# Optimization experiments

Measured on AMD Instinct MI355X. Metric: run time of the kernel, lower is better.

The kernel has to match this reference:

```python
import jax, jax.numpy as jnp
import numpy as np

N_NODES = 50000
N_EDGES = 800000
H_DIM = 128
N_REL2 = 130  # 2 * n_rel with n_rel = 65
BN_EPS = 1e-5


def setup_inputs() -> dict:
    key = jax.random.key(0)
    k1, k2, k3, k4, k5, k6 = jax.random.split(key, 6)
    xavier = float(np.sqrt(2.0 / (H_DIM + H_DIM)))  # xavier_normal_ std for [h,h]
    return {
        "ent_emb": jax.random.normal(k1, (N_NODES, H_DIM), dtype=jnp.float32),
        "rel_emb": jax.random.normal(k2, (N_REL2, H_DIM), dtype=jnp.float32),
        "neigh_w": jax.random.normal(k3, (H_DIM, H_DIM), dtype=jnp.float32) * xavier,
        "gamma": jnp.ones((H_DIM,), dtype=jnp.float32),
        "beta": jnp.zeros((H_DIM,), dtype=jnp.float32),
        "src": jax.random.randint(k4, (N_EDGES,), 0, N_NODES, dtype=jnp.int32),
        "dst": jax.random.randint(k5, (N_EDGES,), 0, N_NODES, dtype=jnp.int32),
        "rel_id": jax.random.randint(k6, (N_EDGES,), 0, N_REL2, dtype=jnp.int32),
    }


def reference(ent_emb, rel_emb, neigh_w, gamma, beta, src, dst, rel_id):
    N = ent_emb.shape[0]
    # u_mul_e: per-edge composition  [E, h]
    comp = ent_emb[src] * rel_emb[rel_id]
    # e_dot_v: per-edge attention logit  [E]
    score = jnp.sum(comp * ent_emb[dst], axis=-1)
    # edge_softmax over incoming edges of each dst node (segment softmax)
    seg_max = jax.ops.segment_max(score, dst, num_segments=N)  # [N]
    ex = jnp.exp(score - seg_max[dst])
    denom = jax.ops.segment_sum(ex, dst, num_segments=N)       # [N]
    alpha = ex / denom[dst]                                     # [E]
    # weighted copy_e + sum aggregation to dst nodes  [N, h]
    neigh = jax.ops.segment_sum(comp * alpha[:, None], dst, num_segments=N)
    # dense epilogue: matmul + BatchNorm1d (training-mode batch stats) + tanh
    h = neigh @ neigh_w
    mu = jnp.mean(h, axis=0)
    var = jnp.mean((h - mu) ** 2, axis=0)  # biased variance, as torch BN uses
    h = (h - mu) / jnp.sqrt(var + BN_EPS) * gamma + beta
    return jnp.tanh(h)
```

## Files before the change

kernel.cpp:

```cpp
#include <hip/hip_runtime.h>
#include <hip/hip_fp16.h>
#include <math.h>

#define N_NODES 50000
#define N_EDGES 800000
#define HD 128
#define BN_EPS 1e-5f

#define SCAN_CHUNK 1024
#define SCAN_NB ((N_NODES + SCAN_CHUNK - 1) / SCAN_CHUNK)

typedef __attribute__((ext_vector_type(8))) _Float16 half8;
typedef __attribute__((ext_vector_type(4))) _Float16 h4;
typedef __attribute__((ext_vector_type(4))) float f32x4;

__device__ __forceinline__ unsigned short f2h(float f) {
  return __half_as_ushort(__float2half(f));
}

__global__ __launch_bounds__(256) void conv_w(const float* __restrict__ W,
                                              unsigned short* __restrict__ Wt) {
  __shared__ float sT[32][33];
  int k0 = (blockIdx.x >> 2) * 32, c0 = (blockIdx.x & 3) * 32;
  int tid = threadIdx.x;
  int kk = tid >> 3, cq = tid & 7;
  float4 v = ((const float4*)W)[(k0 + kk) * 32 + (c0 >> 2) + cq];
  sT[kk][cq * 4 + 0] = v.x;
  sT[kk][cq * 4 + 1] = v.y;
  sT[kk][cq * 4 + 2] = v.z;
  sT[kk][cq * 4 + 3] = v.w;
  __syncthreads();
  int cc = tid >> 3, kq = tid & 7;
  h4 o;
  o.x = (_Float16)sT[kq * 4 + 0][cc];
  o.y = (_Float16)sT[kq * 4 + 1][cc];
  o.z = (_Float16)sT[kq * 4 + 2][cc];
  o.w = (_Float16)sT[kq * 4 + 3][cc];
  ((h4*)(Wt + (c0 + cc) * HD + k0))[kq] = o;
}

__global__ __launch_bounds__(256) void hist(const int* __restrict__ dst,
                                            int* __restrict__ counts,
                                            unsigned short* __restrict__ erank) {
  int i = blockIdx.x * 256 + threadIdx.x;
  if (i >= N_EDGES / 4) return;
  int4 d = ((const int4*)dst)[i];
  ushort4 r;
  r.x = (unsigned short)atomicAdd(counts + d.x, 1);
  r.y = (unsigned short)atomicAdd(counts + d.y, 1);
  r.z = (unsigned short)atomicAdd(counts + d.z, 1);
  r.w = (unsigned short)atomicAdd(counts + d.w, 1);
  ((ushort4*)erank)[i] = r;
}

__global__ __launch_bounds__(256) void scan_blocks(
    const int* __restrict__ buf, int* __restrict__ bsum) {
  int t = threadIdx.x;
  int idx = blockIdx.x * SCAN_CHUNK + t * 4;
  int s = 0;
  if (idx + 3 < N_NODES) {
    int4 v = *(const int4*)(buf + idx);
    s = v.x + v.y + v.z + v.w;
  } else {
#pragma unroll
    for (int j = 0; j < 4; ++j)
      if (idx + j < N_NODES) s += buf[idx + j];
  }
  __shared__ int ls[256];
  ls[t] = s;
  __syncthreads();
  for (int off = 128; off > 0; off >>= 1) {
    if (t < off) ls[t] += ls[t + off];
    __syncthreads();
  }
  if (t == 0) bsum[blockIdx.x] = ls[0];
}

__global__ __launch_bounds__(64) void scan_top(const int* __restrict__ bsum,
                                               int* __restrict__ bbase,
                                               int* buf) {
  int t = threadIdx.x;
  int v = (t < SCAN_NB) ? bsum[t] : 0;
  int incl = v;
#pragma unroll
  for (int off = 1; off < 64; off <<= 1) {
    int u = __shfl_up(incl, off, 64);
    if (t >= off) incl += u;
  }
  if (t < SCAN_NB) bbase[t] = incl - v;
  if (t == 63) buf[N_NODES] = incl;
}

__global__ __launch_bounds__(256) void scan_write(int* buf,
                                                  const int* __restrict__ bbase) {
  int t = threadIdx.x;
  int idx = blockIdx.x * SCAN_CHUNK + t * 4;
  int c[4] = {0, 0, 0, 0};
  if (idx + 3 < N_NODES) {
    int4 v = *(const int4*)(buf + idx);
    c[0] = v.x; c[1] = v.y; c[2] = v.z; c[3] = v.w;
  } else {
#pragma unroll
    for (int j = 0; j < 4; ++j)
      if (idx + j < N_NODES) c[j] = buf[idx + j];
  }
  int s = c[0] + c[1] + c[2] + c[3];
  __shared__ int ls[256];
  ls[t] = s;
  __syncthreads();
  for (int off = 1; off < 256; off <<= 1) {
    int u = (t >= off) ? ls[t - off] : 0;
    __syncthreads();
    ls[t] += u;
    __syncthreads();
  }
  int run = bbase[blockIdx.x] + ls[t] - s;
#pragma unroll
  for (int j = 0; j < 4; ++j) {
    if (idx + j < N_NODES) {
      buf[idx + j] = run;
      run += c[j];
    }
  }
}

__global__ __launch_bounds__(256) void fill_buckets(
    const int* __restrict__ src, const int* __restrict__ dst,
    const int* __restrict__ rid, const unsigned short* __restrict__ erank,
    const int* __restrict__ offsets, int* __restrict__ einfo) {
  int i = blockIdx.x * 256 + threadIdx.x;
  if (i >= N_EDGES / 4) return;
  int4 s4 = ((const int4*)src)[i];
  int4 d4 = ((const int4*)dst)[i];
  int4 r4 = ((const int4*)rid)[i];
  ushort4 k4 = ((const ushort4*)erank)[i];
#pragma unroll
  for (int q = 0; q < 4; ++q) {
    int s = (q == 0) ? s4.x : (q == 1) ? s4.y : (q == 2) ? s4.z : s4.w;
    int d = (q == 0) ? d4.x : (q == 1) ? d4.y : (q == 2) ? d4.z : d4.w;
    int r = (q == 0) ? r4.x : (q == 1) ? r4.y : (q == 2) ? r4.z : r4.w;
    int k = (q == 0) ? k4.x : (q == 1) ? k4.y : (q == 2) ? k4.z : k4.w;
    einfo[offsets[d] + k] = s | (r << 16);
  }
}

__global__ __launch_bounds__(256) void gather_fused(
    const float* __restrict__ ent, const float* __restrict__ rel,
    const int* __restrict__ offsets, const int* __restrict__ einfo,
    unsigned short* __restrict__ scaled_h) {
  int n = blockIdx.x * 4 + (threadIdx.x >> 6);
  if (n >= N_NODES) return;
  int lane = threadIdx.x & 63;
  int half = lane >> 5;
  int l32 = lane & 31;
  int s0 = __builtin_amdgcn_readfirstlane(offsets[n]);
  int s1 = __builtin_amdgcn_readfirstlane(offsets[n + 1]);
  const float4* ent4 = (const float4*)ent;
  const float4* rel4 = (const float4*)rel;
  float4 b = ent4[(long)n * 32 + l32];
  const int* ei = einfo + half;

  float m = -INFINITY, den = 0.f;
  float4 acc = make_float4(0.f, 0.f, 0.f, 0.f);
  int s = s0;
  for (; s + 8 <= s1; s += 8) {
    int w0 = ei[s + 0];
    int w1 = ei[s + 2];
    int w2 = ei[s + 4];
    int w3 = ei[s + 6];
    float4 a0 = ent4[(long)(w0 & 0xFFFF) * 32 + l32];
    float4 c0 = rel4[(w0 >> 16) * 32 + l32];
    float4 a1 = ent4[(long)(w1 & 0xFFFF) * 32 + l32];
    float4 c1 = rel4[(w1 >> 16) * 32 + l32];
    float4 a2 = ent4[(long)(w2 & 0xFFFF) * 32 + l32];
    float4 c2 = rel4[(w2 >> 16) * 32 + l32];
    float4 a3 = ent4[(long)(w3 & 0xFFFF) * 32 + l32];
    float4 c3 = rel4[(w3 >> 16) * 32 + l32];
    float4 q0, q1, q2, q3;
    q0.x = a0.x * c0.x; q0.y = a0.y * c0.y; q0.z = a0.z * c0.z; q0.w = a0.w * c0.w;
    q1.x = a1.x * c1.x; q1.y = a1.y * c1.y; q1.z = a1.z * c1.z; q1.w = a1.w * c1.w;
    q2.x = a2.x * c2.x; q2.y = a2.y * c2.y; q2.z = a2.z * c2.z; q2.w = a2.w * c2.w;
    q3.x = a3.x * c3.x; q3.y = a3.y * c3.y; q3.z = a3.z * c3.z; q3.w = a3.w * c3.w;
    float p0 = q0.x * b.x + q0.y * b.y + q0.z * b.z + q0.w * b.w;
    float p1 = q1.x * b.x + q1.y * b.y + q1.z * b.z + q1.w * b.w;
    float p2 = q2.x * b.x + q2.y * b.y + q2.z * b.z + q2.w * b.w;
    float p3 = q3.x * b.x + q3.y * b.y + q3.z * b.z + q3.w * b.w;
#pragma unroll
    for (int off = 16; off > 0; off >>= 1) {
      p0 += __shfl_xor(p0, off, 64);
      p1 += __shfl_xor(p1, off, 64);
      p2 += __shfl_xor(p2, off, 64);
      p3 += __shfl_xor(p3, off, 64);
    }
    float pm = fmaxf(fmaxf(fmaxf(p0, p1), fmaxf(p2, p3)), m);
    float f = __expf(m - pm);
    float e0 = __expf(p0 - pm);
    float e1 = __expf(p1 - pm);
    float e2 = __expf(p2 - pm);
    float e3 = __expf(p3 - pm);
    den = den * f + ((e0 + e1) + (e2 + e3));
    acc.x = acc.x * f + (q0.x * e0 + q1.x * e1) + (q2.x * e2 + q3.x * e3);
    acc.y = acc.y * f + (q0.y * e0 + q1.y * e1) + (q2.y * e2 + q3.y * e3);
    acc.z = acc.z * f + (q0.z * e0 + q1.z * e1) + (q2.z * e2 + q3.z * e3);
    acc.w = acc.w * f + (q0.w * e0 + q1.w * e1) + (q2.w * e2 + q3.w * e3);
    m = pm;
  }
  for (; s + 2 <= s1; s += 2) {
    int w = ei[s];
    float4 a = ent4[(long)(w & 0xFFFF) * 32 + l32];
    float4 c = rel4[(w >> 16) * 32 + l32];
    float4 q;
    q.x = a.x * c.x; q.y = a.y * c.y; q.z = a.z * c.z; q.w = a.w * c.w;
    float p = q.x * b.x + q.y * b.y + q.z * b.z + q.w * b.w;
#pragma unroll
    for (int off = 16; off > 0; off >>= 1) p += __shfl_xor(p, off, 64);
    float pm = fmaxf(p, m);
    float f = __expf(m - pm);
    float e = __expf(p - pm);
    den = den * f + e;
    acc.x = fmaf(acc.x, f, q.x * e);
    acc.y = fmaf(acc.y, f, q.y * e);
    acc.z = fmaf(acc.z, f, q.z * e);
    acc.w = fmaf(acc.w, f, q.w * e);
    m = pm;
  }
  if (s < s1) {
    int w = einfo[s];
    float4 a = ent4[(long)(w & 0xFFFF) * 32 + l32];
    float4 c = rel4[(w >> 16) * 32 + l32];
    float4 q;
    q.x = a.x * c.x; q.y = a.y * c.y; q.z = a.z * c.z; q.w = a.w * c.w;
    float p = q.x * b.x + q.y * b.y + q.z * b.z + q.w * b.w;
#pragma unroll
    for (int off = 16; off > 0; off >>= 1) p += __shfl_xor(p, off, 64);
    float pn = half ? -INFINITY : p;
    float pm = fmaxf(m, pn);
    float f = (m == -INFINITY) ? 0.f : __expf(m - pm);
    float e = (pn == -INFINITY) ? 0.f : __expf(pn - pm);
    den = den * f + e;
    acc.x = fmaf(acc.x, f, q.x * e);
    acc.y = fmaf(acc.y, f, q.y * e);
    acc.z = fmaf(acc.z, f, q.z * e);
    acc.w = fmaf(acc.w, f, q.w * e);
    m = pm;
  }
  float mo = __shfl_xor(m, 32, 64);
  float deno = __shfl_xor(den, 32, 64);
  float4 acco;
  acco.x = __shfl_xor(acc.x, 32, 64);
  acco.y = __shfl_xor(acc.y, 32, 64);
  acco.z = __shfl_xor(acc.z, 32, 64);
  acco.w = __shfl_xor(acc.w, 32, 64);
  float mm = fmaxf(m, mo);
  float fs = (mm == -INFINITY) ? 0.f : __expf(m - mm);
  float fo = (mm == -INFINITY) ? 0.f : __expf(mo - mm);
  float dtot = den * fs + deno * fo;
  float inv = dtot > 0.f ? 1.f / dtot : 0.f;
  if (half == 0) {
    ushort4 o;
    o.x = f2h((acc.x * fs + acco.x * fo) * inv);
    o.y = f2h((acc.y * fs + acco.y * fo) * inv);
    o.z = f2h((acc.z * fs + acco.z * fo) * inv);
    o.w = f2h((acc.w * fs + acco.w * fo) * inv);
    ((ushort4*)(scaled_h + (long)n * HD))[l32] = o;
  }
}

__global__ __launch_bounds__(256) void gemm_mfma(
    const unsigned short* __restrict__ scaled_h,
    const unsigned short* __restrict__ Wt, float* __restrict__ h,
    float* __restrict__ colsum, float* __restrict__ colsumsq) {
  __shared__ unsigned short sW[128 * 136];
  __shared__ float sStat[256];
  int tid = threadIdx.x;
  int row0 = blockIdx.x * 64;

  for (int i = tid; i < 2048; i += 256) {
    int col = i >> 4, c8 = i & 15;
    *(int4*)&sW[col * 136 + c8 * 8] = ((const int4*)Wt)[i];
  }
  __syncthreads();

  int w = tid >> 6, lane = tid & 63;
  int lrow = lane & 15, lk = lane >> 4;
  int arow = row0 + w * 16 + lrow;
  bool avalid = arow < N_NODES;
  const half8* ap = (const half8*)(scaled_h + (long)(avalid ? arow : 0) * HD);

  f32x4 acc[8];
#pragma unroll
  for (int n = 0; n < 8; ++n) acc[n] = (f32x4){0.f, 0.f, 0.f, 0.f};

#pragma unroll
  for (int kt = 0; kt < 4; ++kt) {
    half8 aF = avalid ? ap[kt * 4 + lk]
                      : (half8){(_Float16)0, (_Float16)0, (_Float16)0, (_Float16)0,
                                (_Float16)0, (_Float16)0, (_Float16)0, (_Float16)0};
#pragma unroll
    for (int n = 0; n < 8; ++n) {
      half8 bF = *(const half8*)&sW[(n * 16 + lrow) * 136 + kt * 32 + lk * 8];
      acc[n] = __builtin_amdgcn_mfma_f32_16x16x32_f16(aF, bF, acc[n], 0, 0, 0);
    }
  }

  float s[8], q[8];
#pragma unroll
  for (int n = 0; n < 8; ++n) {
    int col = n * 16 + lrow;
    s[n] = 0.f;
    q[n] = 0.f;
#pragma unroll
    for (int r = 0; r < 4; ++r) {
      float v = acc[n][r];
      int grow = row0 + w * 16 + lk * 4 + r;
      if (grow < N_NODES) h[(long)grow * HD + col] = v;
      s[n] += v;
      q[n] += v * v;
    }
    s[n] += __shfl_xor(s[n], 16, 64);
    s[n] += __shfl_xor(s[n], 32, 64);
    q[n] += __shfl_xor(q[n], 16, 64);
    q[n] += __shfl_xor(q[n], 32, 64);
  }

  sStat[tid] = 0.f;
  __syncthreads();
  if (lane < 16) {
#pragma unroll
    for (int n = 0; n < 8; ++n) {
      atomicAdd(&sStat[n * 16 + lrow], s[n]);
      atomicAdd(&sStat[128 + n * 16 + lrow], q[n]);
    }
  }
  __syncthreads();
  if (tid < 128) {
    unsafeAtomicAdd(colsum + tid, sStat[tid]);
    unsafeAtomicAdd(colsumsq + tid, sStat[128 + tid]);
  }
}

__global__ __launch_bounds__(256) void bn_tanh(
    float* __restrict__ h, const float* __restrict__ colsum,
    const float* __restrict__ colsumsq, const float* __restrict__ gamma,
    const float* __restrict__ beta) {
  const float invN = 1.f / (float)N_NODES;
  const int total4 = N_NODES * 32;
  for (int i = blockIdx.x * 256 + threadIdx.x; i < total4;
       i += gridDim.x * 256) {
    int c4 = i & 31;
    float4 hv = ((float4*)h)[i];
    float4 S = ((const float4*)colsum)[c4];
    float4 Q = ((const float4*)colsumsq)[c4];
    float4 G = ((const float4*)gamma)[c4];
    float4 B = ((const float4*)beta)[c4];
    float4 o;
    {
      float mu = S.x * invN, var = Q.x * invN - mu * mu;
      o.x = tanhf((hv.x - mu) * rsqrtf(var + BN_EPS) * G.x + B.x);
    }
    {
      float mu = S.y * invN, var = Q.y * invN - mu * mu;
      o.y = tanhf((hv.y - mu) * rsqrtf(var + BN_EPS) * G.y + B.y);
    }
    {
      float mu = S.z * invN, var = Q.z * invN - mu * mu;
      o.z = tanhf((hv.z - mu) * rsqrtf(var + BN_EPS) * G.z + B.z);
    }
    {
      float mu = S.w * invN, var = Q.w * invN - mu * mu;
      o.w = tanhf((hv.w - mu) * rsqrtf(var + BN_EPS) * G.w + B.w);
    }
    ((float4*)h)[i] = o;
  }
}

extern "C" void kernel_launch(void* const* d_in, const int* in_sizes, int n_in,
                              void* d_out, int out_size, void* d_ws, size_t ws_size,
                              hipStream_t stream) {
  const float* ent   = (const float*)d_in[0];
  const float* rel   = (const float*)d_in[1];
  const float* W     = (const float*)d_in[2];
  const float* gamma = (const float*)d_in[3];
  const float* beta  = (const float*)d_in[4];
  const int*   src   = (const int*)d_in[5];
  const int*   dst   = (const int*)d_in[6];
  const int*   rid   = (const int*)d_in[7];
  float* out = (float*)d_out;

  char* ws = (char*)d_ws;
  int* offsets     = (int*)(ws + 0);
  float* colsum    = (float*)(ws + 200064);
  float* colsumsq  = (float*)(ws + 200576);
  int* bsum        = (int*)(ws + 201088);
  int* bbase       = (int*)(ws + 202112);
  unsigned short* Wt = (unsigned short*)(ws + 203136);
  int* einfo         = (int*)(ws + 235904);
  unsigned short* erank    = (unsigned short*)(ws + 3435904);
  unsigned short* scaled_h = (unsigned short*)(ws + 3435904);

  hipMemsetAsync(d_ws, 0, 201088, stream);

  conv_w<<<16, 256, 0, stream>>>(W, Wt);
  hist<<<(N_EDGES / 4 + 255) / 256, 256, 0, stream>>>(dst, offsets, erank);
  scan_blocks<<<SCAN_NB, 256, 0, stream>>>(offsets, bsum);
  scan_top<<<1, 64, 0, stream>>>(bsum, bbase, offsets);
  scan_write<<<SCAN_NB, 256, 0, stream>>>(offsets, bbase);
  fill_buckets<<<(N_EDGES / 4 + 255) / 256, 256, 0, stream>>>(
      src, dst, rid, erank, offsets, einfo);
  gather_fused<<<(N_NODES + 3) / 4, 256, 0, stream>>>(ent, rel, offsets,
                                                      einfo, scaled_h);
  gemm_mfma<<<(N_NODES + 63) / 64, 256, 0, stream>>>(scaled_h, Wt, out,
                                                     colsum, colsumsq);
  bn_tanh<<<2048, 256, 0, stream>>>(out, colsum, colsumsq, gamma, beta);
}
```

Before: 165.6 us.

## Fuse BatchNorm+tanh into GEMM via grid barrier and fold scan_top into scan_write

The GEMM kernel no longer stores the pre-norm matrix. Each block adds its column sums into shared atomics, then all blocks wait at a spin-wait grid barrier on a counter. After the barrier each block applies BatchNorm and tanh to the values still in its registers and writes the final output once. This drops the separate bn_tanh pass and one full read-write of the output. Separately, the top-level scan is recomputed inside every scan_write block, which removes one kernel launch. The grid barrier depends on all 782 blocks being resident at the same time, which is why the launch bound asks for 4 blocks per CU. If they are not all resident it could deadlock, and spinning adds some idle time.

New measurement: 235.8 us. 1.42x slower.

```diff
diff --git a/kernel.cpp b/kernel.cpp
--- a/kernel.cpp
+++ b/kernel.cpp
@@ -9,6 +9,7 @@
 
 #define SCAN_CHUNK 1024
 #define SCAN_NB ((N_NODES + SCAN_CHUNK - 1) / SCAN_CHUNK)
+#define GEMM_NB ((N_NODES + 63) / 64)
 
 typedef __attribute__((ext_vector_type(8))) _Float16 half8;
 typedef __attribute__((ext_vector_type(4))) _Float16 h4;
@@ -76,24 +77,22 @@
   if (t == 0) bsum[blockIdx.x] = ls[0];
 }
 
-__global__ __launch_bounds__(64) void scan_top(const int* __restrict__ bsum,
-                                               int* __restrict__ bbase,
-                                               int* buf) {
+__global__ __launch_bounds__(256) void scan_write(int* buf,
+                                                  const int* __restrict__ bsum) {
+  __shared__ int sBase[SCAN_NB + 1];
   int t = threadIdx.x;
-  int v = (t < SCAN_NB) ? bsum[t] : 0;
-  int incl = v;
-#pragma unroll
-  for (int off = 1; off < 64; off <<= 1) {
-    int u = __shfl_up(incl, off, 64);
-    if (t >= off) incl += u;
-  }
-  if (t < SCAN_NB) bbase[t] = incl - v;
-  if (t == 63) buf[N_NODES] = incl;
-}
-
-__global__ __launch_bounds__(256) void scan_write(int* buf,
-                                                  const int* __restrict__ bbase) {
-  int t = threadIdx.x;
+  if (t < 64) {
+    int v = (t < SCAN_NB) ? bsum[t] : 0;
+    int incl = v;
+#pragma unroll
+    for (int off = 1; off < 64; off <<= 1) {
+      int u = __shfl_up(incl, off, 64);
+      if (t >= off) incl += u;
+    }
+    if (t < SCAN_NB) sBase[t] = incl - v;
+    if (t == 63) sBase[SCAN_NB] = incl;
+  }
+  __syncthreads();
   int idx = blockIdx.x * SCAN_CHUNK + t * 4;
   int c[4] = {0, 0, 0, 0};
   if (idx + 3 < N_NODES) {
@@ -114,7 +113,7 @@
     ls[t] += u;
     __syncthreads();
   }
-  int run = bbase[blockIdx.x] + ls[t] - s;
+  int run = sBase[blockIdx.x] + ls[t] - s;
 #pragma unroll
   for (int j = 0; j < 4; ++j) {
     if (idx + j < N_NODES) {
@@ -122,6 +121,7 @@
       run += c[j];
     }
   }
+  if (blockIdx.x == 0 && t == 0) buf[N_NODES] = sBase[SCAN_NB];
 }
 
 __global__ __launch_bounds__(256) void fill_buckets(
@@ -266,10 +266,12 @@
   }
 }
 
-__global__ __launch_bounds__(256) void gemm_mfma(
+__global__ __launch_bounds__(256, 4) void gemm_bn(
     const unsigned short* __restrict__ scaled_h,
-    const unsigned short* __restrict__ Wt, float* __restrict__ h,
-    float* __restrict__ colsum, float* __restrict__ colsumsq) {
+    const unsigned short* __restrict__ Wt,
+    const float* __restrict__ gamma, const float* __restrict__ beta,
+    float* __restrict__ out, float* __restrict__ colsum,
+    float* __restrict__ colsumsq, int* __restrict__ done) {
   __shared__ unsigned short sW[128 * 136];
   __shared__ float sStat[256];
   int tid = threadIdx.x;
@@ -306,14 +308,12 @@
   float s[8], q[8];
 #pragma unroll
   for (int n = 0; n < 8; ++n) {
-    int col = n * 16 + lrow;
     s[n] = 0.f;
     q[n] = 0.f;
 #pragma unroll
     for (int r = 0; r < 4; ++r) {
-      float v = acc[n][r];
       int grow = row0 + w * 16 + lk * 4 + r;
-      if (grow < N_NODES) h[(long)grow * HD + col] = v;
+      float v = (grow < N_NODES) ? acc[n][r] : 0.f;
       s[n] += v;
       q[n] += v * v;
     }
@@ -337,40 +337,35 @@
     unsafeAtomicAdd(colsum + tid, sStat[tid]);
     unsafeAtomicAdd(colsumsq + tid, sStat[128 + tid]);
   }
-}
-
-__global__ __launch_bounds__(256) void bn_tanh(
-    float* __restrict__ h, const float* __restrict__ colsum,
-    const float* __restrict__ colsumsq, const float* __restrict__ gamma,
-    const float* __restrict__ beta) {
+  __threadfence();
+  __syncthreads();
+  if (tid == 0) {
+    __hip_atomic_fetch_add(done, 1, __ATOMIC_ACQ_REL, __HIP_MEMORY_SCOPE_AGENT);
+    while (__hip_atomic_load(done, __ATOMIC_ACQUIRE, __HIP_MEMORY_SCOPE_AGENT) <
+           (int)gridDim.x) {
+      __builtin_amdgcn_s_sleep(8);
+    }
+  }
+  __syncthreads();
+
   const float invN = 1.f / (float)N_NODES;
-  const int total4 = N_NODES * 32;
-  for (int i = blockIdx.x * 256 + threadIdx.x; i < total4;
-       i += gridDim.x * 256) {
-    int c4 = i & 31;
-    float4 hv = ((float4*)h)[i];
-    float4 S = ((const float4*)colsum)[c4];
-    float4 Q = ((const float4*)colsumsq)[c4];
-    float4 G = ((const float4*)gamma)[c4];
-    float4 B = ((const float4*)beta)[c4];
-    float4 o;
-    {
-      float mu = S.x * invN, var = Q.x * invN - mu * mu;
-      o.x = tanhf((hv.x - mu) * rsqrtf(var + BN_EPS) * G.x + B.x);
-    }
-    {
-      float mu = S.y * invN, var = Q.y * invN - mu * mu;
-      o.y = tanhf((hv.y - mu) * rsqrtf(var + BN_EPS) * G.y + B.y);
-    }
-    {
-      float mu = S.z * invN, var = Q.z * invN - mu * mu;
-      o.z = tanhf((hv.z - mu) * rsqrtf(var + BN_EPS) * G.z + B.z);
-    }
-    {
-      float mu = S.w * invN, var = Q.w * invN - mu * mu;
-      o.w = tanhf((hv.w - mu) * rsqrtf(var + BN_EPS) * G.w + B.w);
-    }
-    ((float4*)h)[i] = o;
+#pragma unroll
+  for (int n = 0; n < 8; ++n) {
+    int col = n * 16 + lrow;
+    float S = __hip_atomic_load(colsum + col, __ATOMIC_RELAXED,
+                                __HIP_MEMORY_SCOPE_AGENT);
+    float Q = __hip_atomic_load(colsumsq + col, __ATOMIC_RELAXED,
+                                __HIP_MEMORY_SCOPE_AGENT);
+    float mu = S * invN;
+    float var = Q * invN - mu * mu;
+    float rinv = rsqrtf(var + BN_EPS);
+    float g = gamma[col], be = beta[col];
+#pragma unroll
+    for (int r = 0; r < 4; ++r) {
+      int grow = row0 + w * 16 + lk * 4 + r;
+      if (grow < N_NODES)
+        out[(long)grow * HD + col] = tanhf((acc[n][r] - mu) * rinv * g + be);
+    }
   }
 }
 
@@ -392,24 +387,22 @@
   float* colsum    = (float*)(ws + 200064);
   float* colsumsq  = (float*)(ws + 200576);
   int* bsum        = (int*)(ws + 201088);
-  int* bbase       = (int*)(ws + 202112);
+  int* done        = (int*)(ws + 202112);
   unsigned short* Wt = (unsigned short*)(ws + 203136);
   int* einfo         = (int*)(ws + 235904);
   unsigned short* erank    = (unsigned short*)(ws + 3435904);
   unsigned short* scaled_h = (unsigned short*)(ws + 3435904);
 
-  hipMemsetAsync(d_ws, 0, 201088, stream);
+  hipMemsetAsync(d_ws, 0, 202240, stream);
 
   conv_w<<<16, 256, 0, stream>>>(W, Wt);
   hist<<<(N_EDGES / 4 + 255) / 256, 256, 0, stream>>>(dst, offsets, erank);
   scan_blocks<<<SCAN_NB, 256, 0, stream>>>(offsets, bsum);
-  scan_top<<<1, 64, 0, stream>>>(bsum, bbase, offsets);
-  scan_write<<<SCAN_NB, 256, 0, stream>>>(offsets, bbase);
+  scan_write<<<SCAN_NB, 256, 0, stream>>>(offsets, bsum);
   fill_buckets<<<(N_EDGES / 4 + 255) / 256, 256, 0, stream>>>(
       src, dst, rid, erank, offsets, einfo);
   gather_fused<<<(N_NODES + 3) / 4, 256, 0, stream>>>(ent, rel, offsets,
                                                       einfo, scaled_h);
-  gemm_mfma<<<(N_NODES + 63) / 64, 256, 0, stream>>>(scaled_h, Wt, out,
-                                                     colsum, colsumsq);
-  bn_tanh<<<2048, 256, 0, stream>>>(out, colsum, colsumsq, gamma, beta);
-}
+  gemm_bn<<<GEMM_NB, 256, 0, stream>>>(scaled_h, Wt, gamma, beta, out,
+                                       colsum, colsumsq, done);
+}
```

## Fold block sums into histogram and use persistent work-stealing gather

Applied to the files above, without the earlier changes.

The histogram kernel now also accumulates per-1024-node bin counts in shared memory and atomically adds them to the block sums. This removes the scan_blocks and scan_top launches, and scan_write now computes the top-level prefix itself. The gather kernel becomes persistent with 2048 blocks, where each wavefront grabs chunks of 8 destination nodes from a global atomic cursor to balance uneven in-degrees. The trade-off is extra atomics and a cursor that must be zeroed by the enlarged memset.

New measurement: 322.3 us. 94.6% more time.

```diff
diff --git a/kernel.cpp b/kernel.cpp
--- a/kernel.cpp
+++ b/kernel.cpp
@@ -9,6 +9,7 @@
 
 #define SCAN_CHUNK 1024
 #define SCAN_NB ((N_NODES + SCAN_CHUNK - 1) / SCAN_CHUNK)
+#define GCHUNK 8
 
 typedef __attribute__((ext_vector_type(8))) _Float16 half8;
 typedef __attribute__((ext_vector_type(4))) _Float16 h4;
@@ -41,59 +42,49 @@
 
 __global__ __launch_bounds__(256) void hist(const int* __restrict__ dst,
                                             int* __restrict__ counts,
-                                            unsigned short* __restrict__ erank) {
-  int i = blockIdx.x * 256 + threadIdx.x;
-  if (i >= N_EDGES / 4) return;
-  int4 d = ((const int4*)dst)[i];
-  ushort4 r;
-  r.x = (unsigned short)atomicAdd(counts + d.x, 1);
-  r.y = (unsigned short)atomicAdd(counts + d.y, 1);
-  r.z = (unsigned short)atomicAdd(counts + d.z, 1);
-  r.w = (unsigned short)atomicAdd(counts + d.w, 1);
-  ((ushort4*)erank)[i] = r;
-}
-
-__global__ __launch_bounds__(256) void scan_blocks(
-    const int* __restrict__ buf, int* __restrict__ bsum) {
+                                            unsigned short* __restrict__ erank,
+                                            int* __restrict__ bsum) {
+  __shared__ int sBin[SCAN_NB];
+  int tid = threadIdx.x;
+  if (tid < SCAN_NB) sBin[tid] = 0;
+  __syncthreads();
+  int i = blockIdx.x * 256 + tid;
+  if (i < N_EDGES / 4) {
+    int4 d = ((const int4*)dst)[i];
+    ushort4 r;
+    r.x = (unsigned short)atomicAdd(counts + d.x, 1);
+    r.y = (unsigned short)atomicAdd(counts + d.y, 1);
+    r.z = (unsigned short)atomicAdd(counts + d.z, 1);
+    r.w = (unsigned short)atomicAdd(counts + d.w, 1);
+    ((ushort4*)erank)[i] = r;
+    atomicAdd(&sBin[d.x >> 10], 1);
+    atomicAdd(&sBin[d.y >> 10], 1);
+    atomicAdd(&sBin[d.z >> 10], 1);
+    atomicAdd(&sBin[d.w >> 10], 1);
+  }
+  __syncthreads();
+  if (tid < SCAN_NB) {
+    int v = sBin[tid];
+    if (v) atomicAdd(bsum + tid, v);
+  }
+}
+
+__global__ __launch_bounds__(256) void scan_write(int* buf,
+                                                  const int* __restrict__ bsum) {
+  __shared__ int sBase[SCAN_NB + 1];
   int t = threadIdx.x;
-  int idx = blockIdx.x * SCAN_CHUNK + t * 4;
-  int s = 0;
-  if (idx + 3 < N_NODES) {
-    int4 v = *(const int4*)(buf + idx);
-    s = v.x + v.y + v.z + v.w;
-  } else {
-#pragma unroll
-    for (int j = 0; j < 4; ++j)
-      if (idx + j < N_NODES) s += buf[idx + j];
-  }
-  __shared__ int ls[256];
-  ls[t] = s;
-  __syncthreads();
-  for (int off = 128; off > 0; off >>= 1) {
-    if (t < off) ls[t] += ls[t + off];
-    __syncthreads();
-  }
-  if (t == 0) bsum[blockIdx.x] = ls[0];
-}
-
-__global__ __launch_bounds__(64) void scan_top(const int* __restrict__ bsum,
-                                               int* __restrict__ bbase,
-                                               int* buf) {
-  int t = threadIdx.x;
-  int v = (t < SCAN_NB) ? bsum[t] : 0;
-  int incl = v;
-#pragma unroll
-  for (int off = 1; off < 64; off <<= 1) {
-    int u = __shfl_up(incl, off, 64);
-    if (t >= off) incl += u;
-  }
-  if (t < SCAN_NB) bbase[t] = incl - v;
-  if (t == 63) buf[N_NODES] = incl;
-}
-
-__global__ __launch_bounds__(256) void scan_write(int* buf,
-                                                  const int* __restrict__ bbase) {
-  int t = threadIdx.x;
+  if (t < 64) {
+    int v = (t < SCAN_NB) ? bsum[t] : 0;
+    int incl = v;
+#pragma unroll
+    for (int off = 1; off < 64; off <<= 1) {
+      int u = __shfl_up(incl, off, 64);
+      if (t >= off) incl += u;
+    }
+    if (t < SCAN_NB) sBase[t] = incl - v;
+    if (t == 63) sBase[SCAN_NB] = incl;
+  }
+  __syncthreads();
   int idx = blockIdx.x * SCAN_CHUNK + t * 4;
   int c[4] = {0, 0, 0, 0};
   if (idx + 3 < N_NODES) {
@@ -114,7 +105,7 @@
     ls[t] += u;
     __syncthreads();
   }
-  int run = bbase[blockIdx.x] + ls[t] - s;
+  int run = sBase[blockIdx.x] + ls[t] - s;
 #pragma unroll
   for (int j = 0; j < 4; ++j) {
     if (idx + j < N_NODES) {
@@ -122,6 +113,7 @@
       run += c[j];
     }
   }
+  if (blockIdx.x == 0 && t == 0) buf[N_NODES] = sBase[SCAN_NB];
 }
 
 __global__ __launch_bounds__(256) void fill_buckets(
@@ -147,122 +139,129 @@
 __global__ __launch_bounds__(256) void gather_fused(
     const float* __restrict__ ent, const float* __restrict__ rel,
     const int* __restrict__ offsets, const int* __restrict__ einfo,
-    unsigned short* __restrict__ scaled_h) {
-  int n = blockIdx.x * 4 + (threadIdx.x >> 6);
-  if (n >= N_NODES) return;
+    unsigned short* __restrict__ scaled_h, int* __restrict__ cursor) {
   int lane = threadIdx.x & 63;
   int half = lane >> 5;
   int l32 = lane & 31;
-  int s0 = __builtin_amdgcn_readfirstlane(offsets[n]);
-  int s1 = __builtin_amdgcn_readfirstlane(offsets[n + 1]);
   const float4* ent4 = (const float4*)ent;
   const float4* rel4 = (const float4*)rel;
-  float4 b = ent4[(long)n * 32 + l32];
   const int* ei = einfo + half;
 
-  float m = -INFINITY, den = 0.f;
-  float4 acc = make_float4(0.f, 0.f, 0.f, 0.f);
-  int s = s0;
-  for (; s + 8 <= s1; s += 8) {
-    int w0 = ei[s + 0];
-    int w1 = ei[s + 2];
-    int w2 = ei[s + 4];
-    int w3 = ei[s + 6];
-    float4 a0 = ent4[(long)(w0 & 0xFFFF) * 32 + l32];
-    float4 c0 = rel4[(w0 >> 16) * 32 + l32];
-    float4 a1 = ent4[(long)(w1 & 0xFFFF) * 32 + l32];
-    float4 c1 = rel4[(w1 >> 16) * 32 + l32];
-    float4 a2 = ent4[(long)(w2 & 0xFFFF) * 32 + l32];
-    float4 c2 = rel4[(w2 >> 16) * 32 + l32];
-    float4 a3 = ent4[(long)(w3 & 0xFFFF) * 32 + l32];
-    float4 c3 = rel4[(w3 >> 16) * 32 + l32];
-    float4 q0, q1, q2, q3;
-    q0.x = a0.x * c0.x; q0.y = a0.y * c0.y; q0.z = a0.z * c0.z; q0.w = a0.w * c0.w;
-    q1.x = a1.x * c1.x; q1.y = a1.y * c1.y; q1.z = a1.z * c1.z; q1.w = a1.w * c1.w;
-    q2.x = a2.x * c2.x; q2.y = a2.y * c2.y; q2.z = a2.z * c2.z; q2.w = a2.w * c2.w;
-    q3.x = a3.x * c3.x; q3.y = a3.y * c3.y; q3.z = a3.z * c3.z; q3.w = a3.w * c3.w;
-    float p0 = q0.x * b.x + q0.y * b.y + q0.z * b.z + q0.w * b.w;
-    float p1 = q1.x * b.x + q1.y * b.y + q1.z * b.z + q1.w * b.w;
-    float p2 = q2.x * b.x + q2.y * b.y + q2.z * b.z + q2.w * b.w;
-    float p3 = q3.x * b.x + q3.y * b.y + q3.z * b.z + q3.w * b.w;
-#pragma unroll
-    for (int off = 16; off > 0; off >>= 1) {
-      p0 += __shfl_xor(p0, off, 64);
-      p1 += __shfl_xor(p1, off, 64);
-      p2 += __shfl_xor(p2, off, 64);
-      p3 += __shfl_xor(p3, off, 64);
-    }
-    float pm = fmaxf(fmaxf(fmaxf(p0, p1), fmaxf(p2, p3)), m);
-    float f = __expf(m - pm);
-    float e0 = __expf(p0 - pm);
-    float e1 = __expf(p1 - pm);
-    float e2 = __expf(p2 - pm);
-    float e3 = __expf(p3 - pm);
-    den = den * f + ((e0 + e1) + (e2 + e3));
-    acc.x = acc.x * f + (q0.x * e0 + q1.x * e1) + (q2.x * e2 + q3.x * e3);
-    acc.y = acc.y * f + (q0.y * e0 + q1.y * e1) + (q2.y * e2 + q3.y * e3);
-    acc.z = acc.z * f + (q0.z * e0 + q1.z * e1) + (q2.z * e2 + q3.z * e3);
-    acc.w = acc.w * f + (q0.w * e0 + q1.w * e1) + (q2.w * e2 + q3.w * e3);
-    m = pm;
-  }
-  for (; s + 2 <= s1; s += 2) {
-    int w = ei[s];
-    float4 a = ent4[(long)(w & 0xFFFF) * 32 + l32];
-    float4 c = rel4[(w >> 16) * 32 + l32];
-    float4 q;
-    q.x = a.x * c.x; q.y = a.y * c.y; q.z = a.z * c.z; q.w = a.w * c.w;
-    float p = q.x * b.x + q.y * b.y + q.z * b.z + q.w * b.w;
-#pragma unroll
-    for (int off = 16; off > 0; off >>= 1) p += __shfl_xor(p, off, 64);
-    float pm = fmaxf(p, m);
-    float f = __expf(m - pm);
-    float e = __expf(p - pm);
-    den = den * f + e;
-    acc.x = fmaf(acc.x, f, q.x * e);
-    acc.y = fmaf(acc.y, f, q.y * e);
-    acc.z = fmaf(acc.z, f, q.z * e);
-    acc.w = fmaf(acc.w, f, q.w * e);
-    m = pm;
-  }
-  if (s < s1) {
-    int w = einfo[s];
-    float4 a = ent4[(long)(w & 0xFFFF) * 32 + l32];
-    float4 c = rel4[(w >> 16) * 32 + l32];
-    float4 q;
-    q.x = a.x * c.x; q.y = a.y * c.y; q.z = a.z * c.z; q.w = a.w * c.w;
-    float p = q.x * b.x + q.y * b.y + q.z * b.z + q.w * b.w;
-#pragma unroll
-    for (int off = 16; off > 0; off >>= 1) p += __shfl_xor(p, off, 64);
-    float pn = half ? -INFINITY : p;
-    float pm = fmaxf(m, pn);
-    float f = (m == -INFINITY) ? 0.f : __expf(m - pm);
-    float e = (pn == -INFINITY) ? 0.f : __expf(pn - pm);
-    den = den * f + e;
-    acc.x = fmaf(acc.x, f, q.x * e);
-    acc.y = fmaf(acc.y, f, q.y * e);
-    acc.z = fmaf(acc.z, f, q.z * e);
-    acc.w = fmaf(acc.w, f, q.w * e);
-    m = pm;
-  }
-  float mo = __shfl_xor(m, 32, 64);
-  float deno = __shfl_xor(den, 32, 64);
-  float4 acco;
-  acco.x = __shfl_xor(acc.x, 32, 64);
-  acco.y = __shfl_xor(acc.y, 32, 64);
-  acco.z = __shfl_xor(acc.z, 32, 64);
-  acco.w = __shfl_xor(acc.w, 32, 64);
-  float mm = fmaxf(m, mo);
-  float fs = (mm == -INFINITY) ? 0.f : __expf(m - mm);
-  float fo = (mm == -INFINITY) ? 0.f : __expf(mo - mm);
-  float dtot = den * fs + deno * fo;
-  float inv = dtot > 0.f ? 1.f / dtot : 0.f;
-  if (half == 0) {
-    ushort4 o;
-    o.x = f2h((acc.x * fs + acco.x * fo) * inv);
-    o.y = f2h((acc.y * fs + acco.y * fo) * inv);
-    o.z = f2h((acc.z * fs + acco.z * fo) * inv);
-    o.w = f2h((acc.w * fs + acco.w * fo) * inv);
-    ((ushort4*)(scaled_h + (long)n * HD))[l32] = o;
+  for (;;) {
+    int base = 0;
+    if (lane == 0) base = atomicAdd(cursor, GCHUNK);
+    base = __shfl(base, 0, 64);
+    if (base >= N_NODES) return;
+    int nend = min(base + GCHUNK, N_NODES);
+    for (int n = base; n < nend; ++n) {
+      int s0 = __builtin_amdgcn_readfirstlane(offsets[n]);
+      int s1 = __builtin_amdgcn_readfirstlane(offsets[n + 1]);
+      float4 b = ent4[(long)n * 32 + l32];
+      float m = -INFINITY, den = 0.f;
+      float4 acc = make_float4(0.f, 0.f, 0.f, 0.f);
+      int s = s0;
+      for (; s + 8 <= s1; s += 8) {
+        int w0 = ei[s + 0];
+        int w1 = ei[s + 2];
+        int w2 = ei[s + 4];
+        int w3 = ei[s + 6];
+        float4 a0 = ent4[(long)(w0 & 0xFFFF) * 32 + l32];
+        float4 c0 = rel4[(w0 >> 16) * 32 + l32];
+        float4 a1 = ent4[(long)(w1 & 0xFFFF) * 32 + l32];
+        float4 c1 = rel4[(w1 >> 16) * 32 + l32];
+        float4 a2 = ent4[(long)(w2 & 0xFFFF) * 32 + l32];
+        float4 c2 = rel4[(w2 >> 16) * 32 + l32];
+        float4 a3 = ent4[(long)(w3 & 0xFFFF) * 32 + l32];
+        float4 c3 = rel4[(w3 >> 16) * 32 + l32];
+        float4 q0, q1, q2, q3;
+        q0.x = a0.x * c0.x; q0.y = a0.y * c0.y; q0.z = a0.z * c0.z; q0.w = a0.w * c0.w;
+        q1.x = a1.x * c1.x; q1.y = a1.y * c1.y; q1.z = a1.z * c1.z; q1.w = a1.w * c1.w;
+        q2.x = a2.x * c2.x; q2.y = a2.y * c2.y; q2.z = a2.z * c2.z; q2.w = a2.w * c2.w;
+        q3.x = a3.x * c3.x; q3.y = a3.y * c3.y; q3.z = a3.z * c3.z; q3.w = a3.w * c3.w;
+        float p0 = q0.x * b.x + q0.y * b.y + q0.z * b.z + q0.w * b.w;
+        float p1 = q1.x * b.x + q1.y * b.y + q1.z * b.z + q1.w * b.w;
+        float p2 = q2.x * b.x + q2.y * b.y + q2.z * b.z + q2.w * b.w;
+        float p3 = q3.x * b.x + q3.y * b.y + q3.z * b.z + q3.w * b.w;
+#pragma unroll
+        for (int off = 16; off > 0; off >>= 1) {
+          p0 += __shfl_xor(p0, off, 64);
+          p1 += __shfl_xor(p1, off, 64);
+          p2 += __shfl_xor(p2, off, 64);
+          p3 += __shfl_xor(p3, off, 64);
+        }
+        float pm = fmaxf(fmaxf(fmaxf(p0, p1), fmaxf(p2, p3)), m);
+        float f = __expf(m - pm);
+        float e0 = __expf(p0 - pm);
+        float e1 = __expf(p1 - pm);
+        float e2 = __expf(p2 - pm);
+        float e3 = __expf(p3 - pm);
+        den = den * f + ((e0 + e1) + (e2 + e3));
+        acc.x = acc.x * f + (q0.x * e0 + q1.x * e1) + (q2.x * e2 + q3.x * e3);
+        acc.y = acc.y * f + (q0.y * e0 + q1.y * e1) + (q2.y * e2 + q3.y * e3);
+        acc.z = acc.z * f + (q0.z * e0 + q1.z * e1) + (q2.z * e2 + q3.z * e3);
+        acc.w = acc.w * f + (q0.w * e0 + q1.w * e1) + (q2.w * e2 + q3.w * e3);
+        m = pm;
+      }
+      for (; s + 2 <= s1; s += 2) {
+        int w = ei[s];
+        float4 a = ent4[(long)(w & 0xFFFF) * 32 + l32];
+        float4 c = rel4[(w >> 16) * 32 + l32];
+        float4 q;
+        q.x = a.x * c.x; q.y = a.y * c.y; q.z = a.z * c.z; q.w = a.w * c.w;
+        float p = q.x * b.x + q.y * b.y + q.z * b.z + q.w * b.w;
+#pragma unroll
+        for (int off = 16; off > 0; off >>= 1) p += __shfl_xor(p, off, 64);
+        float pm = fmaxf(p, m);
+        float f = __expf(m - pm);
+        float e = __expf(p - pm);
+        den = den * f + e;
+        acc.x = fmaf(acc.x, f, q.x * e);
+        acc.y = fmaf(acc.y, f, q.y * e);
+        acc.z = fmaf(acc.z, f, q.z * e);
+        acc.w = fmaf(acc.w, f, q.w * e);
+        m = pm;
+      }
+      if (s < s1) {
+        int w = einfo[s];
+        float4 a = ent4[(long)(w & 0xFFFF) * 32 + l32];
+        float4 c = rel4[(w >> 16) * 32 + l32];
+        float4 q;
+        q.x = a.x * c.x; q.y = a.y * c.y; q.z = a.z * c.z; q.w = a.w * c.w;
+        float p = q.x * b.x + q.y * b.y + q.z * b.z + q.w * b.w;
+#pragma unroll
+        for (int off = 16; off > 0; off >>= 1) p += __shfl_xor(p, off, 64);
+        float pn = half ? -INFINITY : p;
+        float pm = fmaxf(m, pn);
+        float f = (m == -INFINITY) ? 0.f : __expf(m - pm);
+        float e = (pn == -INFINITY) ? 0.f : __expf(pn - pm);
+        den = den * f + e;
+        acc.x = fmaf(acc.x, f, q.x * e);
+        acc.y = fmaf(acc.y, f, q.y * e);
+        acc.z = fmaf(acc.z, f, q.z * e);
+        acc.w = fmaf(acc.w, f, q.w * e);
+        m = pm;
+      }
+      float mo = __shfl_xor(m, 32, 64);
+      float deno = __shfl_xor(den, 32, 64);
+      float4 acco;
+      acco.x = __shfl_xor(acc.x, 32, 64);
+      acco.y = __shfl_xor(acc.y, 32, 64);
+      acco.z = __shfl_xor(acc.z, 32, 64);
+      acco.w = __shfl_xor(acc.w, 32, 64);
+      float mm = fmaxf(m, mo);
+      float fs = (mm == -INFINITY) ? 0.f : __expf(m - mm);
+      float fo = (mm == -INFINITY) ? 0.f : __expf(mo - mm);
+      float dtot = den * fs + deno * fo;
+      float inv = dtot > 0.f ? 1.f / dtot : 0.f;
+      if (half == 0) {
+        ushort4 o;
+        o.x = f2h((acc.x * fs + acco.x * fo) * inv);
+        o.y = f2h((acc.y * fs + acco.y * fo) * inv);
+        o.z = f2h((acc.z * fs + acco.z * fo) * inv);
+        o.w = f2h((acc.w * fs + acco.w * fo) * inv);
+        ((ushort4*)(scaled_h + (long)n * HD))[l32] = o;
+      }
+    }
   }
 }
 
@@ -392,23 +391,21 @@
   float* colsum    = (float*)(ws + 200064);
   float* colsumsq  = (float*)(ws + 200576);
   int* bsum        = (int*)(ws + 201088);
-  int* bbase       = (int*)(ws + 202112);
+  int* cursor      = (int*)(ws + 202112);
   unsigned short* Wt = (unsigned short*)(ws + 203136);
   int* einfo         = (int*)(ws + 235904);
   unsigned short* erank    = (unsigned short*)(ws + 3435904);
   unsigned short* scaled_h = (unsigned short*)(ws + 3435904);
 
-  hipMemsetAsync(d_ws, 0, 201088, stream);
+  hipMemsetAsync(d_ws, 0, 202240, stream);
 
   conv_w<<<16, 256, 0, stream>>>(W, Wt);
-  hist<<<(N_EDGES / 4 + 255) / 256, 256, 0, stream>>>(dst, offsets, erank);
-  scan_blocks<<<SCAN_NB, 256, 0, stream>>>(offsets, bsum);
-  scan_top<<<1, 64, 0, stream>>>(bsum, bbase, offsets);
-  scan_write<<<SCAN_NB, 256, 0, stream>>>(offsets, bbase);
+  hist<<<(N_EDGES / 4 + 255) / 256, 256, 0, stream>>>(dst, offsets, erank, bsum);
+  scan_write<<<SCAN_NB, 256, 0, stream>>>(offsets, bsum);
   fill_buckets<<<(N_EDGES / 4 + 255) / 256, 256, 0, stream>>>(
       src, dst, rid, erank, offsets, einfo);
-  gather_fused<<<(N_NODES + 3) / 4, 256, 0, stream>>>(ent, rel, offsets,
-                                                      einfo, scaled_h);
+  gather_fused<<<2048, 256, 0, stream>>>(ent, rel, offsets, einfo, scaled_h,
+                                         cursor);
   gemm_mfma<<<(N_NODES + 63) / 64, 256, 0, stream>>>(scaled_h, Wt, out,
                                                      colsum, colsumsq);
   bn_tanh<<<2048, 256, 0, stream>>>(out, colsum, colsumsq, gamma, beta);
```
